# Kernel optimization log

Measured on AMD Instinct MI355X. Metric: run time of the kernel, lower is better.

Reference implementation:

```python
import jax, jax.numpy as jnp
import numpy as np

N_NODES = 50000
N_EDGES = 800000
D_IN, D_HID, N_CLS = 128, 64, 40


def setup_inputs() -> dict:
    key = jax.random.key(0)
    ks = jax.random.split(key, 12)
    x = jax.random.normal(ks[0], (N_NODES, D_IN), dtype=jnp.float32)
    edge_index = jax.random.randint(ks[1], (2, N_EDGES), 0, N_NODES, dtype=jnp.int64)
    s = 0.05
    return {
        "x": x,
        "edge_index": edge_index,
        # layer 1 params
        "W1": jax.random.normal(ks[2], (D_IN, D_HID), dtype=jnp.float32) * s,
        "aW1": jax.random.normal(ks[3], (2 * D_HID, 1), dtype=jnp.float32) * s,
        "ab1": jnp.zeros((1,), dtype=jnp.float32),
        "b1": jnp.zeros((D_HID,), dtype=jnp.float32),
        # layer 2 params
        "W2": jax.random.normal(ks[4], (D_HID, D_HID), dtype=jnp.float32) * s,
        "aW2": jax.random.normal(ks[5], (2 * D_HID, 1), dtype=jnp.float32) * s,
        "ab2": jnp.zeros((1,), dtype=jnp.float32),
        "b2": jnp.zeros((D_HID,), dtype=jnp.float32),
        # output head
        "Wo": jax.random.normal(ks[6], (D_HID, N_CLS), dtype=jnp.float32) * s,
        "bo": jnp.zeros((N_CLS,), dtype=jnp.float32),
    }


def _gat_layer(x, src, dst, W, aW, ab, bias, n_nodes):
    h = x @ W                                    # [N, out]
    s = h[src]                                   # [E, out] gather source feats
    t = h[dst]                                   # [E, out] gather target feats
    # per-edge attention score, leaky_relu(negative_slope=0.2)
    sim = jax.nn.leaky_relu(jnp.concatenate([s, t], axis=-1) @ aW + ab,
                            negative_slope=0.2)[:, 0]        # [E]
    # scatter-softmax over incoming edges of each dst node
    m = jax.ops.segment_max(sim, dst, num_segments=n_nodes)   # [N]
    e = jnp.exp(sim - m[dst])
    z = jax.ops.segment_sum(e, dst, num_segments=n_nodes)     # [N]
    a = e / z[dst]                                             # [E]
    msg = a[:, None] * s                                       # [E, out]
    out = jax.ops.segment_max(msg, dst, num_segments=n_nodes)  # scatter-max aggr
    return out + bias


def reference(x, edge_index, W1, aW1, ab1, b1, W2, aW2, ab2, b2, Wo, bo):
    n = x.shape[0]
    loop = jnp.arange(n, dtype=edge_index.dtype)
    src = jnp.concatenate([edge_index[0], loop])  # add self loops
    dst = jnp.concatenate([edge_index[1], loop])
    h = jax.nn.relu(_gat_layer(x, src, dst, W1, aW1, ab1, b1, n))
    h = jax.nn.relu(_gat_layer(h, src, dst, W2, aW2, ab2, b2, n))
    logits = h @ Wo + bo
    return jax.nn.log_softmax(logits, axis=-1)
```

## Files before the change

kernel.cpp:

```cpp
#include <hip/hip_runtime.h>
#include <hip/hip_fp16.h>
#include <math.h>

#define N_NODES 50000
#define N_EDGES 800000
#define E_TOT   (N_EDGES + N_NODES)
#define D_HID   64
#define N_CLS   40
#define SCAN_B  256
#define N_CHUNKS ((N_NODES + SCAN_B - 1) / SCAN_B)
#define NB      391
#define EPB     4096

struct __align__(8) H4 { __half2 a, b; };

typedef short bf16x8 __attribute__((ext_vector_type(8)));
typedef float f32x4  __attribute__((ext_vector_type(4)));

__device__ __forceinline__ unsigned pk_max_f16(unsigned a, unsigned b) {
    unsigned r;
    asm("v_pk_max_f16 %0, %1, %2" : "=v"(r) : "v"(a), "v"(b));
    return r;
}
__device__ __forceinline__ unsigned pk_mul_f16(unsigned a, unsigned b) {
    unsigned r;
    asm("v_pk_mul_f16 %0, %1, %2" : "=v"(r) : "v"(a), "v"(b));
    return r;
}
__device__ __forceinline__ unsigned pkmax_xor(unsigned v, int o) {
    unsigned t = __shfl_xor((int)v, o, 64);
    return pk_max_f16(v, t);
}

__device__ __forceinline__ unsigned short f2bf(float f) {
    unsigned u = __float_as_uint(f);
    u += 0x7FFFu + ((u >> 16) & 1);
    return (unsigned short)(u >> 16);
}
__device__ __forceinline__ unsigned pk_bf(float a, float b) {
    return (unsigned)f2bf(a) | ((unsigned)f2bf(b) << 16);
}

__global__ void k_convert(const void* ei, int2* __restrict__ pairs,
                          int* __restrict__ deg) {
    __shared__ int s_is32;
    if (threadIdx.x == 0) s_is32 = 0;
    __syncthreads();
    const int* p32 = (const int*)ei;
    if (p32[2 * threadIdx.x + 1] != 0) atomicOr(&s_is32, 1);
    __syncthreads();
    int e = blockIdx.x * 256 + threadIdx.x;
    if (e >= N_EDGES) return;
    int s, d;
    if (s_is32) {
        s = p32[e]; d = p32[N_EDGES + e];
    } else {
        const long long* p64 = (const long long*)ei;
        s = (int)p64[e]; d = (int)p64[N_EDGES + e];
    }
    pairs[e] = make_int2(s, d);
    atomicAdd(&deg[d], 1);
}

__device__ __forceinline__ int block_scan_incl(int v, int* wsum) {
    int lane = threadIdx.x & 63, w = threadIdx.x >> 6;
    int s = v;
#pragma unroll
    for (int d = 1; d < 64; d <<= 1) {
        int t = __shfl_up(s, d, 64);
        if (lane >= d) s += t;
    }
    if (lane == 63) wsum[w] = s;
    __syncthreads();
    int add = 0;
    for (int ww = 0; ww < (threadIdx.x >> 6); ++ww) add += wsum[ww];
    return s + add;
}

__global__ void k_scan1(const int* __restrict__ deg, int* __restrict__ rowptr,
                        int* __restrict__ partials) {
    __shared__ int wsum[4];
    int i = blockIdx.x * SCAN_B + threadIdx.x;
    int v = (i < N_NODES) ? deg[i] + 1 : 0;
    int s = block_scan_incl(v, wsum);
    if (i < N_NODES) rowptr[i] = s - v;
    if (threadIdx.x == SCAN_B - 1) partials[blockIdx.x] = s;
}

__global__ void k_scan2(int* partials) {
    __shared__ int wsum[4];
    int i = threadIdx.x;
    int v = (i < N_CHUNKS) ? partials[i] : 0;
    int s = block_scan_incl(v, wsum);
    if (i < N_CHUNKS) partials[i] = s - v;
}

__global__ void k_scan3(const int* __restrict__ partials, int* __restrict__ rowptr) {
    int i = blockIdx.x * SCAN_B + threadIdx.x;
    if (i < N_NODES) rowptr[i] += partials[blockIdx.x];
    if (blockIdx.x == 0 && threadIdx.x == 0) rowptr[N_NODES] = E_TOT;
}

__global__ void k_bucket_init(const int* __restrict__ rowptr, int* __restrict__ bcursor) {
    int b = threadIdx.x;
    if (b < NB) bcursor[b] = rowptr[b << 7] - (b << 7);
}

__global__ __launch_bounds__(256) void k_bucket_scatter(
        const int2* __restrict__ pairs_in, int* __restrict__ bcursor,
        int2* __restrict__ pairs_bkt) {
    __shared__ int counts[512];
    __shared__ int gbase[512];
    int t = threadIdx.x;
    counts[t] = 0; counts[t + 256] = 0;
    __syncthreads();
    int base = blockIdx.x * EPB;
    int nEdge = min(EPB, N_EDGES - base);
    int2 pr0, pr1, pr2, pr3, pr4, pr5, pr6, pr7, pr8, pr9, prA, prB, prC, prD, prE, prF;
    int rk[16], bk[16];
#define LOADI(i, pv) { int idx = t + (i) * 256;                        \
        if (idx < nEdge) { pv = pairs_in[base + idx];                   \
            bk[i] = pv.y >> 7; rk[i] = atomicAdd(&counts[bk[i]], 1); } }
    LOADI(0, pr0) LOADI(1, pr1) LOADI(2, pr2) LOADI(3, pr3)
    LOADI(4, pr4) LOADI(5, pr5) LOADI(6, pr6) LOADI(7, pr7)
    LOADI(8, pr8) LOADI(9, pr9) LOADI(10, prA) LOADI(11, prB)
    LOADI(12, prC) LOADI(13, prD) LOADI(14, prE) LOADI(15, prF)
#undef LOADI
    __syncthreads();
    if (counts[t])       gbase[t]       = atomicAdd(&bcursor[t], counts[t]);
    if (counts[t + 256]) gbase[t + 256] = atomicAdd(&bcursor[t + 256], counts[t + 256]);
    __syncthreads();
#define STOREI(i, pv) { int idx = t + (i) * 256;                        \
        if (idx < nEdge) pairs_bkt[gbase[bk[i]] + rk[i]] = pv; }
    STOREI(0, pr0) STOREI(1, pr1) STOREI(2, pr2) STOREI(3, pr3)
    STOREI(4, pr4) STOREI(5, pr5) STOREI(6, pr6) STOREI(7, pr7)
    STOREI(8, pr8) STOREI(9, pr9) STOREI(10, prA) STOREI(11, prB)
    STOREI(12, prC) STOREI(13, prD) STOREI(14, prE) STOREI(15, prF)
#undef STOREI
}

__global__ __launch_bounds__(256) void k_bucket_place(
        const int2* __restrict__ pairs_bkt, const int* __restrict__ rowptr,
        int* __restrict__ src_sorted) {
    __shared__ int cur[128];
    int b = blockIdx.x, t = threadIdx.x;
    int d0 = b << 7;
    int dEnd = min(d0 + 128, N_NODES);
    if (t < 128) {
        int d = d0 + t;
        if (d < dEnd) {
            int r = rowptr[d];
            src_sorted[r] = d;
            cur[t] = r + 1;
        }
    }
    __syncthreads();
    int pbase = rowptr[d0] - d0;
    int pend  = rowptr[dEnd] - dEnd;
    for (int idx = pbase + t; idx < pend; idx += 256) {
        int2 p = pairs_bkt[idx];
        int pos = atomicAdd(&cur[p.y - d0], 1);
        src_sorted[pos] = p.x;
    }
}

template<int K>
__global__ __launch_bounds__(256) void k_gemm_alpha(
        const float* __restrict__ x, const float* __restrict__ W,
        const float* __restrict__ aW,
        H4* __restrict__ WhH,
        float* __restrict__ alpha_s, float* __restrict__ alpha_t) {
    __shared__ unsigned short xb[64][K + 8];
    __shared__ unsigned short wt[64][K + 8];
    int tid = threadIdx.x;
    int rowBase = blockIdx.x * 64;

    {
        int rr = tid >> 2;
        int kc = (tid & 3) * (K / 4);
        const float* xr = x + (size_t)min(rowBase + rr, N_NODES - 1) * K + kc;
        unsigned* dst = (unsigned*)&xb[rr][kc];
#pragma unroll
        for (int j = 0; j < K / 4; j += 8) {
            float4 v0 = *(const float4*)(xr + j);
            float4 v1 = *(const float4*)(xr + j + 4);
            dst[j / 2 + 0] = pk_bf(v0.x, v0.y);
            dst[j / 2 + 1] = pk_bf(v0.z, v0.w);
            dst[j / 2 + 2] = pk_bf(v1.x, v1.y);
            dst[j / 2 + 3] = pk_bf(v1.z, v1.w);
        }
    }
    for (int i = tid; i < K * 64; i += 256) {
        int k = i >> 6, n = i & 63;
        wt[n][k] = f2bf(W[i]);
    }
    __syncthreads();

    int w = tid >> 6, lane = tid & 63;
    int la = lane & 15, hi = lane >> 4;

    f32x4 acc[4];
#pragma unroll
    for (int c = 0; c < 4; ++c) acc[c] = (f32x4){0.f, 0.f, 0.f, 0.f};

#pragma unroll
    for (int t = 0; t < K / 32; ++t) {
        int k0 = t * 32 + hi * 8;
        bf16x8 af = *(const bf16x8*)&xb[w * 16 + la][k0];
#pragma unroll
        for (int c = 0; c < 4; ++c) {
            bf16x8 bfr = *(const bf16x8*)&wt[c * 16 + la][k0];
            acc[c] = __builtin_amdgcn_mfma_f32_16x16x32_bf16(af, bfr, acc[c], 0, 0, 0);
        }
    }

    float as4[4], at4[4];
#pragma unroll
    for (int c = 0; c < 4; ++c) {
        as4[c] = aW[c * 16 + la];
        at4[c] = aW[64 + c * 16 + la];
    }
#pragma unroll
    for (int r = 0; r < 4; ++r) {
        int row = rowBase + w * 16 + hi * 4 + r;
        float ps = acc[0][r] * as4[0] + acc[1][r] * as4[1]
                 + acc[2][r] * as4[2] + acc[3][r] * as4[3];
        float pt = acc[0][r] * at4[0] + acc[1][r] * at4[1]
                 + acc[2][r] * at4[2] + acc[3][r] * at4[3];
#pragma unroll
        for (int o = 1; o < 16; o <<= 1) {
            ps += __shfl_xor(ps, o, 64);
            pt += __shfl_xor(pt, o, 64);
        }
        if (row < N_NODES) {
            __half* wr = (__half*)&WhH[(size_t)row * 16];
#pragma unroll
            for (int c = 0; c < 4; ++c)
                wr[c * 16 + la] = __float2half(acc[c][r]);
            if (la == 0) { alpha_s[row] = ps; alpha_t[row] = pt; }
        }
    }
}

__device__ void slow_node(int rs, int re, const int* __restrict__ src_sorted,
                          const float* __restrict__ alpha_s, float at,
                          const H4* __restrict__ WhH, int lane, int fl2,
                          float& z, unsigned vm[4]) {
    float m = -INFINITY;
    for (int base = rs; base < re; base += 64) {
        int idx = base + lane;
        float sim = -INFINITY;
        if (idx < re) {
            int sv = src_sorted[idx];
            float t = alpha_s[sv] + at;
            sim = t > 0.f ? t : 0.2f * t;
        }
#pragma unroll
        for (int o = 32; o; o >>= 1) sim = fmaxf(sim, __shfl_xor(sim, o, 64));
        m = fmaxf(m, sim);
    }
    z = 0.f;
    float vsc = -INFINITY;
    for (int base = rs; base < re; base += 64) {
        int idx = base + lane;
        int cnt = min(64, re - base);
        int svv = 0;
        float ev = 0.f;
        if (idx < re) {
            svv = src_sorted[idx];
            float t = alpha_s[svv] + at;
            t = t > 0.f ? t : 0.2f * t;
            ev = __expf(t - m);
        }
        float sz = ev;
#pragma unroll
        for (int o = 32; o; o >>= 1) sz += __shfl_xor(sz, o, 64);
        z += sz;
        for (int j = 0; j < cnt; ++j) {
            int sj = __shfl(svv, j, 64);
            float ej = __shfl(ev, j, 64);
            float v = __half2float(((const __half*)WhH)[(size_t)sj * 64 + lane]);
            vsc = fmaxf(vsc, ej * v);
        }
    }
#pragma unroll
    for (int q = 0; q < 4; ++q) {
        float a0 = __shfl(vsc, fl2 * 8 + 2 * q, 64);
        float a1 = __shfl(vsc, fl2 * 8 + 2 * q + 1, 64);
        __half2 p = __floats2half2_rn(a0, a1);
        vm[q] = *(unsigned*)&p;
    }
}

template<int HEAD>
__global__ void k_node_aggr(const int* __restrict__ rowptr, const int* __restrict__ src_sorted,
                            const float* __restrict__ alpha_s, const float* __restrict__ alpha_t,
                            const float* __restrict__ ab, const H4* __restrict__ WhH,
                            const float* __restrict__ bias,
                            const float* __restrict__ Wo, const float* __restrict__ bo,
                            float* __restrict__ outp) {
    __shared__ float sWo[HEAD ? 64 * N_CLS : 1];
    __shared__ float sh[HEAD ? 8 * 64 : 1];
    int lane = threadIdx.x, w = threadIdx.y;
    if (HEAD) {
        int tid = w * 64 + lane;
        for (int i = tid; i < 64 * N_CLS; i += 256) sWo[i] = Wo[i];
    }
    int dA = blockIdx.x * 8 + w * 2;
    int dB = dA + 1;
    int rsA = rowptr[dA], reA = rowptr[dA + 1];
    int rsB = rowptr[dB], reB = rowptr[dB + 1];
    int degA = reA - rsA, degB = reB - rsB;
    float abv = ab[0];
    float atA = alpha_t[dA] + abv;
    float atB = alpha_t[dB] + abv;
    int g2 = lane >> 3, fl2 = lane & 7;
    const char* whb = (const char*)WhH;

    float zA, zB;
    unsigned vmA[4], vmB[4];

    if (degA <= 64 && degB <= 64) {
        int svA = src_sorted[rsA + min(lane, degA - 1)];
        int svB = src_sorted[rsB + min(lane, degB - 1)];
        float tA = alpha_s[svA] + atA; tA = tA > 0.f ? tA : 0.2f * tA;
        float tB = alpha_s[svB] + atB; tB = tB > 0.f ? tB : 0.2f * tB;
        float evA = __expf(tA);
        float evB = __expf(tB);
        float zzA = (lane < degA) ? evA : 0.f;
        float zzB = (lane < degB) ? evB : 0.f;
#pragma unroll
        for (int o = 32; o; o >>= 1) {
            zzA += __shfl_xor(zzA, o, 64);
            zzB += __shfl_xor(zzB, o, 64);
        }
        zA = zzA; zB = zzB;
        int ofsA = svA * 128, ofsB = svB * 128;

        const unsigned NEGINF2 = 0xFC00FC00u;
        unsigned vA0 = NEGINF2, vA1 = NEGINF2, vA2 = NEGINF2, vA3 = NEGINF2;
        unsigned vB0 = NEGINF2, vB1 = NEGINF2, vB2 = NEGINF2, vB3 = NEGINF2;
#define ROUND(ev, ofs, deg, v0, v1, v2, v3, r) { \
        int j = (r) * 8 + g2; j = j < (deg) ? j : (deg) - 1;              \
        float ej = __shfl((ev), j, 64);                                   \
        int ro = __shfl((ofs), j, 64);                                    \
        uint4 hv = *(const uint4*)(whb + ro + fl2 * 16);                  \
        __half2 ejh = __float2half2_rn(ej);                               \
        unsigned ej2 = *(unsigned*)&ejh;                                  \
        v0 = pk_max_f16(v0, pk_mul_f16(ej2, hv.x));                       \
        v1 = pk_max_f16(v1, pk_mul_f16(ej2, hv.y));                       \
        v2 = pk_max_f16(v2, pk_mul_f16(ej2, hv.z));                       \
        v3 = pk_max_f16(v3, pk_mul_f16(ej2, hv.w)); }
#define RA(r) ROUND(evA, ofsA, degA, vA0, vA1, vA2, vA3, r)
#define RB(r) ROUND(evB, ofsB, degB, vB0, vB1, vB2, vB3, r)

        RA(0) RB(0) RA(1) RB(1)
        if (degA > 16) { RA(2) RA(3) }
        if (degB > 16) { RB(2) RB(3) }
        if (degA > 32) { RA(4) RA(5) RA(6) RA(7) }
        if (degB > 32) { RB(4) RB(5) RB(6) RB(7) }
#undef RA
#undef RB
#undef ROUND
#pragma unroll
        for (int o = 8; o <= 32; o <<= 1) {
            vA0 = pkmax_xor(vA0, o); vA1 = pkmax_xor(vA1, o);
            vA2 = pkmax_xor(vA2, o); vA3 = pkmax_xor(vA3, o);
            vB0 = pkmax_xor(vB0, o); vB1 = pkmax_xor(vB1, o);
            vB2 = pkmax_xor(vB2, o); vB3 = pkmax_xor(vB3, o);
        }
        vmA[0] = vA0; vmA[1] = vA1; vmA[2] = vA2; vmA[3] = vA3;
        vmB[0] = vB0; vmB[1] = vB1; vmB[2] = vB2; vmB[3] = vB3;
    } else {
        slow_node(rsA, reA, src_sorted, alpha_s, atA, WhH, lane, fl2, zA, vmA);
        slow_node(rsB, reB, src_sorted, alpha_s, atB, WhH, lane, fl2, zB, vmB);
    }

    float4 b0 = *(const float4*)(bias + fl2 * 8);
    float4 b1 = *(const float4*)(bias + fl2 * 8 + 4);
    float rzA = 1.0f / zA, rzB = 1.0f / zB;
    float h8A[8], h8B[8];
#pragma unroll
    for (int q = 0; q < 4; ++q) {
        float2 fa = __half22float2(*(__half2*)&vmA[q]);
        float2 fb = __half22float2(*(__half2*)&vmB[q]);
        h8A[2 * q] = fa.x; h8A[2 * q + 1] = fa.y;
        h8B[2 * q] = fb.x; h8B[2 * q + 1] = fb.y;
    }
    float bias8[8] = { b0.x, b0.y, b0.z, b0.w, b1.x, b1.y, b1.z, b1.w };
#pragma unroll
    for (int q = 0; q < 8; ++q) {
        h8A[q] = fmaxf(h8A[q] * rzA + bias8[q], 0.f);
        h8B[q] = fmaxf(h8B[q] * rzB + bias8[q], 0.f);
    }

    if (!HEAD) {
        if (g2 == 0) {
            float* op = outp + (size_t)dA * 64 + fl2 * 8;
            *(float4*)op = make_float4(h8A[0], h8A[1], h8A[2], h8A[3]);
            *(float4*)(op + 4) = make_float4(h8A[4], h8A[5], h8A[6], h8A[7]);
        } else if (g2 == 1) {
            float* op = outp + (size_t)dB * 64 + fl2 * 8;
            *(float4*)op = make_float4(h8B[0], h8B[1], h8B[2], h8B[3]);
            *(float4*)(op + 4) = make_float4(h8B[4], h8B[5], h8B[6], h8B[7]);
        }
    } else {
        if (g2 == 0) {
            float* sp = sh + (2 * w) * 64 + fl2 * 8;
            *(float4*)sp = make_float4(h8A[0], h8A[1], h8A[2], h8A[3]);
            *(float4*)(sp + 4) = make_float4(h8A[4], h8A[5], h8A[6], h8A[7]);
        } else if (g2 == 1) {
            float* sp = sh + (2 * w + 1) * 64 + fl2 * 8;
            *(float4*)sp = make_float4(h8B[0], h8B[1], h8B[2], h8B[3]);
            *(float4*)(sp + 4) = make_float4(h8B[4], h8B[5], h8B[6], h8B[7]);
        }
        __syncthreads();
#pragma unroll
        for (int n = 0; n < 2; ++n) {
            int dd = dA + n;
            const float* hrow = sh + (2 * w + n) * 64;
            float logit = -INFINITY;
            if (lane < N_CLS) {
                float acc = bo[lane];
#pragma unroll
                for (int k = 0; k < 64; ++k)
                    acc = fmaf(hrow[k], sWo[k * N_CLS + lane], acc);
                logit = acc;
            }
            float mx = logit;
#pragma unroll
            for (int o = 32; o; o >>= 1) mx = fmaxf(mx, __shfl_xor(mx, o, 64));
            float ex = (lane < N_CLS) ? __expf(logit - mx) : 0.f;
            float sm = ex;
#pragma unroll
            for (int o = 32; o; o >>= 1) sm += __shfl_xor(sm, o, 64);
            float lse = mx + __logf(sm);
            if (lane < N_CLS) outp[(size_t)dd * N_CLS + lane] = logit - lse;
        }
    }
}

extern "C" void kernel_launch(void* const* d_in, const int* in_sizes, int n_in,
                              void* d_out, int out_size, void* d_ws, size_t ws_size,
                              hipStream_t stream) {
    const float* x   = (const float*)d_in[0];
    const void*  ei  = d_in[1];
    const float* W1  = (const float*)d_in[2];
    const float* aW1 = (const float*)d_in[3];
    const float* ab1 = (const float*)d_in[4];
    const float* b1  = (const float*)d_in[5];
    const float* W2  = (const float*)d_in[6];
    const float* aW2 = (const float*)d_in[7];
    const float* ab2 = (const float*)d_in[8];
    const float* b2  = (const float*)d_in[9];
    const float* Wo  = (const float*)d_in[10];
    const float* bo  = (const float*)d_in[11];
    float* out = (float*)d_out;

    char* ws = (char*)d_ws;
    size_t off = 0;
    auto alloc = [&](size_t bytes) {
        void* p = ws + off;
        off += (bytes + 255) & ~(size_t)255;
        return p;
    };
    int2*  pairs      = (int2*)alloc((size_t)N_EDGES * 8);
    int2*  pairs_bkt  = (int2*)alloc((size_t)N_EDGES * 8);
    int*   deg        = (int*)alloc((size_t)N_NODES * 4);
    int*   rowptr     = (int*)alloc((size_t)(N_NODES + 1) * 4);
    int*   bcursor    = (int*)alloc((size_t)512 * 4);
    int*   partials   = (int*)alloc((size_t)SCAN_B * 4);
    int*   src_sorted = (int*)alloc((size_t)E_TOT * 4);
    H4*    WhH        = (H4*)alloc((size_t)N_NODES * 64 * 2);
    float* h_mid      = (float*)alloc((size_t)N_NODES * 64 * 4);
    float* alpha_s    = (float*)alloc((size_t)N_NODES * 4);
    float* alpha_t    = (float*)alloc((size_t)N_NODES * 4);

    const int B = 256;
    int gEdgeE = (N_EDGES + B - 1) / B;
    int gPassC = (N_EDGES + EPB - 1) / EPB;
    dim3 blk2(64, 4);
    int gRow  = N_NODES / 8;
    int gGemm = (N_NODES + 63) / 64;

    hipMemsetAsync(deg, 0, (size_t)N_NODES * 4, stream);
    k_convert<<<gEdgeE, B, 0, stream>>>(ei, pairs, deg);
    k_scan1<<<N_CHUNKS, SCAN_B, 0, stream>>>(deg, rowptr, partials);
    k_scan2<<<1, SCAN_B, 0, stream>>>(partials);
    k_scan3<<<N_CHUNKS, SCAN_B, 0, stream>>>(partials, rowptr);
    k_bucket_init<<<1, 512, 0, stream>>>(rowptr, bcursor);
    k_bucket_scatter<<<gPassC, B, 0, stream>>>(pairs, bcursor, pairs_bkt);
    k_bucket_place<<<NB, B, 0, stream>>>(pairs_bkt, rowptr, src_sorted);

    k_gemm_alpha<128><<<gGemm, 256, 0, stream>>>(x, W1, aW1, WhH, alpha_s, alpha_t);
    k_node_aggr<0><<<gRow, blk2, 0, stream>>>(rowptr, src_sorted, alpha_s, alpha_t,
                                              ab1, WhH, b1, nullptr, nullptr, h_mid);

    k_gemm_alpha<64><<<gGemm, 256, 0, stream>>>(h_mid, W2, aW2, WhH, alpha_s, alpha_t);
    k_node_aggr<1><<<gRow, blk2, 0, stream>>>(rowptr, src_sorted, alpha_s, alpha_t,
                                              ab2, WhH, b2, Wo, bo, out);
}
```

Measured before the change: 162.9 us.

## Fuse edge conversion into layer-1 GEMM and merge scan finalize kernels

Moves edge-index conversion and degree counting into the first GEMM+alpha kernel, with each of the 782 GEMM blocks handling 1024 edges, so one launch does both jobs. It also merges scan2, scan3 and bucket_init into a single k_scan_fin kernel in which every block redundantly scans the chunk partials. Together these remove three kernel launches and shorten the serial chain. The costs are redundant partial scans in every block and extra work inside the GEMM kernel.

New measurement: 157.4 us. 1.04x faster.

```diff
diff --git a/kernel.cpp b/kernel.cpp
--- a/kernel.cpp
+++ b/kernel.cpp
@@ -11,6 +11,7 @@
 #define N_CHUNKS ((N_NODES + SCAN_B - 1) / SCAN_B)
 #define NB      391
 #define EPB     4096
+#define EPG     1024
 
 struct __align__(8) H4 { __half2 a, b; };
 
@@ -39,27 +40,6 @@
 }
 __device__ __forceinline__ unsigned pk_bf(float a, float b) {
     return (unsigned)f2bf(a) | ((unsigned)f2bf(b) << 16);
-}
-
-__global__ void k_convert(const void* ei, int2* __restrict__ pairs,
-                          int* __restrict__ deg) {
-    __shared__ int s_is32;
-    if (threadIdx.x == 0) s_is32 = 0;
-    __syncthreads();
-    const int* p32 = (const int*)ei;
-    if (p32[2 * threadIdx.x + 1] != 0) atomicOr(&s_is32, 1);
-    __syncthreads();
-    int e = blockIdx.x * 256 + threadIdx.x;
-    if (e >= N_EDGES) return;
-    int s, d;
-    if (s_is32) {
-        s = p32[e]; d = p32[N_EDGES + e];
-    } else {
-        const long long* p64 = (const long long*)ei;
-        s = (int)p64[e]; d = (int)p64[N_EDGES + e];
-    }
-    pairs[e] = make_int2(s, d);
-    atomicAdd(&deg[d], 1);
 }
 
 __device__ __forceinline__ int block_scan_incl(int v, int* wsum) {
@@ -87,23 +67,25 @@
     if (threadIdx.x == SCAN_B - 1) partials[blockIdx.x] = s;
 }
 
-__global__ void k_scan2(int* partials) {
+__global__ void k_scan_fin(const int* __restrict__ partials, int* __restrict__ rowptr,
+                           int* __restrict__ bcursor) {
+    __shared__ int sp[SCAN_B];
     __shared__ int wsum[4];
-    int i = threadIdx.x;
-    int v = (i < N_CHUNKS) ? partials[i] : 0;
+    int t = threadIdx.x, b = blockIdx.x;
+    int v = (t < N_CHUNKS) ? partials[t] : 0;
     int s = block_scan_incl(v, wsum);
-    if (i < N_CHUNKS) partials[i] = s - v;
-}
-
-__global__ void k_scan3(const int* __restrict__ partials, int* __restrict__ rowptr) {
-    int i = blockIdx.x * SCAN_B + threadIdx.x;
-    if (i < N_NODES) rowptr[i] += partials[blockIdx.x];
-    if (blockIdx.x == 0 && threadIdx.x == 0) rowptr[N_NODES] = E_TOT;
-}
-
-__global__ void k_bucket_init(const int* __restrict__ rowptr, int* __restrict__ bcursor) {
-    int b = threadIdx.x;
-    if (b < NB) bcursor[b] = rowptr[b << 7] - (b << 7);
+    sp[t] = s - v;
+    __syncthreads();
+    int add = sp[b];
+    int i = b * SCAN_B + t;
+    int r = 0;
+    if (i < N_NODES) {
+        r = rowptr[i] + add;
+        rowptr[i] = r;
+    }
+    if (b == 0 && t == 0) rowptr[N_NODES] = E_TOT;
+    if (t == 0)   bcursor[2 * b]     = r - ((2 * b) << 7);
+    if (t == 128 && i < N_NODES) bcursor[2 * b + 1] = r - ((2 * b + 1) << 7);
 }
 
 __global__ __launch_bounds__(256) void k_bucket_scatter(
@@ -164,14 +146,16 @@
     }
 }
 
-template<int K>
+template<int K, int DOCONV>
 __global__ __launch_bounds__(256) void k_gemm_alpha(
         const float* __restrict__ x, const float* __restrict__ W,
         const float* __restrict__ aW,
         H4* __restrict__ WhH,
-        float* __restrict__ alpha_s, float* __restrict__ alpha_t) {
+        float* __restrict__ alpha_s, float* __restrict__ alpha_t,
+        const void* ei, int2* __restrict__ pairs, int* __restrict__ deg) {
     __shared__ unsigned short xb[64][K + 8];
     __shared__ unsigned short wt[64][K + 8];
+    __shared__ int s_is32;
     int tid = threadIdx.x;
     int rowBase = blockIdx.x * 64;
 
@@ -194,6 +178,7 @@
         int k = i >> 6, n = i & 63;
         wt[n][k] = f2bf(W[i]);
     }
+    if (DOCONV && tid == 0) s_is32 = 0;
     __syncthreads();
 
     int w = tid >> 6, lane = tid & 63;
@@ -238,6 +223,29 @@
             for (int c = 0; c < 4; ++c)
                 wr[c * 16 + la] = __float2half(acc[c][r]);
             if (la == 0) { alpha_s[row] = ps; alpha_t[row] = pt; }
+        }
+    }
+
+    if (DOCONV) {
+        const int* p32 = (const int*)ei;
+        if (p32[2 * tid + 1] != 0) atomicOr(&s_is32, 1);
+        __syncthreads();
+        int is32 = s_is32;
+        int base = blockIdx.x * EPG;
+#pragma unroll
+        for (int i = 0; i < EPG / 256; ++i) {
+            int e = base + tid + i * 256;
+            if (e < N_EDGES) {
+                int s, d;
+                if (is32) {
+                    s = p32[e]; d = p32[N_EDGES + e];
+                } else {
+                    const long long* p64 = (const long long*)ei;
+                    s = (int)p64[e]; d = (int)p64[N_EDGES + e];
+                }
+                pairs[e] = make_int2(s, d);
+                atomicAdd(&deg[d], 1);
+            }
         }
     }
 }
@@ -477,26 +485,25 @@
     float* alpha_t    = (float*)alloc((size_t)N_NODES * 4);
 
     const int B = 256;
-    int gEdgeE = (N_EDGES + B - 1) / B;
     int gPassC = (N_EDGES + EPB - 1) / EPB;
     dim3 blk2(64, 4);
     int gRow  = N_NODES / 8;
     int gGemm = (N_NODES + 63) / 64;
 
     hipMemsetAsync(deg, 0, (size_t)N_NODES * 4, stream);
-    k_convert<<<gEdgeE, B, 0, stream>>>(ei, pairs, deg);
+
+    k_gemm_alpha<128, 1><<<gGemm, 256, 0, stream>>>(x, W1, aW1, WhH, alpha_s, alpha_t,
+                                                    ei, pairs, deg);
     k_scan1<<<N_CHUNKS, SCAN_B, 0, stream>>>(deg, rowptr, partials);
-    k_scan2<<<1, SCAN_B, 0, stream>>>(partials);
-    k_scan3<<<N_CHUNKS, SCAN_B, 0, stream>>>(partials, rowptr);
-    k_bucket_init<<<1, 512, 0, stream>>>(rowptr, bcursor);
+    k_scan_fin<<<N_CHUNKS, SCAN_B, 0, stream>>>(partials, rowptr, bcursor);
     k_bucket_scatter<<<gPassC, B, 0, stream>>>(pairs, bcursor, pairs_bkt);
     k_bucket_place<<<NB, B, 0, stream>>>(pairs_bkt, rowptr, src_sorted);
 
-    k_gemm_alpha<128><<<gGemm, 256, 0, stream>>>(x, W1, aW1, WhH, alpha_s, alpha_t);
     k_node_aggr<0><<<gRow, blk2, 0, stream>>>(rowptr, src_sorted, alpha_s, alpha_t,
                                               ab1, WhH, b1, nullptr, nullptr, h_mid);
 
-    k_gemm_alpha<64><<<gGemm, 256, 0, stream>>>(h_mid, W2, aW2, WhH, alpha_s, alpha_t);
+    k_gemm_alpha<64, 0><<<gGemm, 256, 0, stream>>>(h_mid, W2, aW2, WhH, alpha_s, alpha_t,
+                                                   nullptr, nullptr, nullptr);
     k_node_aggr<1><<<gRow, blk2, 0, stream>>>(rowptr, src_sorted, alpha_s, alpha_t,
                                               ab2, WhH, b2, Wo, bo, out);
 }
```
